# Optimization experiments

Hardware: AMD Instinct MI355X
Metric: run time of the kernel (lower is better)

Reference implementation:

```python
import jax, jax.numpy as jnp
import numpy as np

B, L, H = 2, 2048, 2048
DI, N, DTR, K = 4096, 16, 128, 4  # intermediate, state, dt_rank, conv kernel


def setup_inputs() -> dict:
    key = jax.random.key(0)
    ks = jax.random.split(key, 8)
    x = jax.random.normal(ks[0], (B, L, H), jnp.float32)
    in_proj_w = jax.random.normal(ks[1], (2 * DI, H), jnp.float32) * 0.02
    conv1d_w = jax.random.normal(ks[2], (DI, 1, K), jnp.float32) * 0.1
    conv1d_b = jnp.zeros((DI,), jnp.float32)
    x_proj_w = jax.random.normal(ks[3], (DTR + 2 * N, DI), jnp.float32) * 0.02
    bound = DTR ** -0.5
    dt_proj_w = jax.random.uniform(ks[4], (DI, DTR), jnp.float32, -bound, bound)
    # faithful dt bias init: inverse-softplus of dt ~ Uniform-log[0.001, 0.1]
    dt = jnp.exp(jax.random.uniform(ks[5], (DI,), jnp.float32)
                 * (np.log(0.1) - np.log(0.001)) + np.log(0.001))
    dt = jnp.clip(dt, 1e-4)
    dt_proj_b = dt + jnp.log(-jnp.expm1(-dt))
    A_log = jnp.log(jnp.broadcast_to(jnp.arange(1, N + 1, dtype=jnp.float32), (DI, N)))
    D = jnp.ones((DI,), jnp.float32)
    out_proj_w = jax.random.normal(ks[6], (H, DI), jnp.float32) * 0.02
    return dict(x=x, in_proj_w=in_proj_w, conv1d_w=conv1d_w, conv1d_b=conv1d_b,
                x_proj_w=x_proj_w, dt_proj_w=dt_proj_w, dt_proj_b=dt_proj_b,
                A_log=A_log, D=D, out_proj_w=out_proj_w)


def _mamba_forward(x, in_proj_w, conv1d_w, conv1d_b, x_proj_w,
                   dt_proj_w, dt_proj_b, A_log, D, out_proj_w):
    # in_proj -> split into ssm input and gate (res)
    x_and_res = jnp.einsum('blh,eh->ble', x, in_proj_w)          # [B,L,2*DI]
    xi, res = jnp.split(x_and_res, 2, axis=-1)                    # [B,L,DI] each

    # depthwise causal conv1d (kernel K, left-pad K-1, truncated to L)
    xc = jnp.transpose(xi, (0, 2, 1))                             # [B,DI,L]
    xc = jax.lax.conv_general_dilated(
        xc, conv1d_w, window_strides=(1,), padding=((K - 1, 0),),
        dimension_numbers=('NCH', 'OIH', 'NCH'), feature_group_count=DI)
    xc = xc + conv1d_b[None, :, None]
    u = jax.nn.silu(jnp.transpose(xc, (0, 2, 1)))                 # [B,L,DI]

    # selective SSM parameters
    A = -jnp.exp(A_log.astype(jnp.float32))                       # [DI,N]
    x_dbl = jnp.einsum('bld,ed->ble', u, x_proj_w)                # [B,L,DTR+2N]
    dlt, Bm, Cm = jnp.split(x_dbl, [DTR, DTR + N], axis=-1)
    delta = jax.nn.softplus(jnp.einsum('blr,dr->bld', dlt, dt_proj_w) + dt_proj_b)

    # selective scan over time; carry h: [B,DI,N]
    def step(h, inp):
        d_t, B_t, C_t, u_t = inp                                  # [B,DI],[B,N],[B,N],[B,DI]
        dA = jnp.exp(d_t[:, :, None] * A)                         # [B,DI,N]
        h = dA * h + d_t[:, :, None] * B_t[:, None, :] * u_t[:, :, None]
        y_t = jnp.einsum('bdn,bn->bd', h, C_t)
        return h, y_t

    xs = (jnp.transpose(delta, (1, 0, 2)), jnp.transpose(Bm, (1, 0, 2)),
          jnp.transpose(Cm, (1, 0, 2)), jnp.transpose(u, (1, 0, 2)))
    h0 = jnp.zeros((x.shape[0], DI, N), jnp.float32)
    _, ys = jax.lax.scan(step, h0, xs)                            # ys: [L,B,DI]
    y = jnp.transpose(ys, (1, 0, 2)) + u * D.astype(jnp.float32)  # skip via D

    y = y * jax.nn.silu(res)                                      # gate
    return jnp.einsum('bld,hd->blh', y, out_proj_w)               # [B,L,H]


def reference(x, in_proj_w, conv1d_w, conv1d_b, x_proj_w,
              dt_proj_w, dt_proj_b, A_log, D, out_proj_w):
    return _mamba_forward(x, in_proj_w, conv1d_w, conv1d_b, x_proj_w,
                          dt_proj_w, dt_proj_b, A_log, D, out_proj_w)
```

## Files before the change

### kernel.cpp

```cpp
#include <hip/hip_runtime.h>
#include <hip/hip_bf16.h>
#include <stdint.h>

#define DEV static __device__ __forceinline__

typedef __attribute__((ext_vector_type(8))) short short8;
typedef __attribute__((ext_vector_type(4))) float f32x4;
typedef __attribute__((address_space(3))) void lds_void;
typedef __attribute__((address_space(1))) void glb_void;

constexpr int CB = 2, CL = 2048, CH = 2048, CDI = 4096, CN = 16, CDTR = 128;
constexpr int BLR = CB * CL;
constexpr int NC = 32, LC = 64;
constexpr int KSL = 8;

DEV ushort f2b(float f) {
  union { float f; uint32_t u; } v; v.f = f;
  uint32_t u = v.u;
  return (ushort)((u + 0x7fffu + ((u >> 16) & 1u)) >> 16);
}
DEV float b2f(ushort b) {
  union { uint32_t u; float f; } v; v.u = ((uint32_t)b) << 16;
  return v.f;
}
DEV void gload16(const ushort* g, ushort* l) {
  __builtin_amdgcn_global_load_lds((const glb_void*)g, (lds_void*)l, 16, 0, 0);
}
DEV f32x4 mfma16(short8 a, short8 b, f32x4 c) {
  return __builtin_amdgcn_mfma_f32_16x16x32_bf16(a, b, c, 0, 0, 0);
}

__global__ void cast_kernel(const float* __restrict__ in, ushort* __restrict__ out, int n4) {
  int i = blockIdx.x * blockDim.x + threadIdx.x;
  if (i >= n4) return;
  float4 v = *(const float4*)(in + (size_t)i * 4);
  *(ushort4*)(out + (size_t)i * 4) = make_ushort4(f2b(v.x), f2b(v.y), f2b(v.z), f2b(v.w));
}

__global__ void cast_pad_xproj_kernel(const float* __restrict__ in, ushort* __restrict__ out) {
  int i = blockIdx.x * blockDim.x + threadIdx.x;
  if (i >= (256 * 4096 / 4)) return;
  int idx = i * 4;
  int r = idx >> 12;
  ushort4 o;
  if (r < 160) {
    float4 v = *(const float4*)(in + idx);
    o = make_ushort4(f2b(v.x), f2b(v.y), f2b(v.z), f2b(v.w));
  } else {
    o = make_ushort4(0, 0, 0, 0);
  }
  *(ushort4*)(out + idx) = o;
}

__global__ void conv_silu_kernel(const ushort* __restrict__ xr, const float* __restrict__ w,
                                 const float* __restrict__ bias, ushort* __restrict__ u) {
  int t = blockIdx.x * blockDim.x + threadIdx.x;
  if (t >= BLR * CDI / 2) return;
  int d2 = t & (CDI / 2 - 1);
  int bl = t >> 11;
  int l = bl & (CL - 1);
  int d = d2 << 1;
  float4 w0 = *(const float4*)(w + (size_t)d * 4);
  float4 w1 = *(const float4*)(w + (size_t)d * 4 + 4);
  float wa0[4] = {w0.x, w0.y, w0.z, w0.w};
  float wa1[4] = {w1.x, w1.y, w1.z, w1.w};
  float a0 = bias[d], a1 = bias[d + 1];
#pragma unroll
  for (int k = 0; k < 4; ++k) {
    int ls = l - 3 + k;
    if (ls >= 0) {
      ushort2 xv = *(const ushort2*)(xr + (size_t)(bl - 3 + k) * 8192 + d);
      a0 = fmaf(wa0[k], b2f(xv.x), a0);
      a1 = fmaf(wa1[k], b2f(xv.y), a1);
    }
  }
  float s0 = a0 / (1.f + __expf(-a0));
  float s1 = a1 / (1.f + __expf(-a1));
  *(ushort2*)(u + (size_t)bl * 4096 + d) = make_ushort2(f2b(s0), f2b(s1));
}

template<int EPI>
__global__ __launch_bounds__(256, 4)
void gemm_bt_kernel(const ushort* __restrict__ A, const ushort* __restrict__ Bw,
                    void* __restrict__ Cp, const float* __restrict__ bias,
                    int M, int N, int K) {
  __shared__ ushort sA[128 * 32];
  __shared__ ushort sB[128 * 32];
  const int tid = threadIdx.x;
  const int bm = blockIdx.x, bn = blockIdx.y;
  const int w = tid >> 6, l = tid & 63;
  const int wr = w >> 1, wc = w & 1;
  const int q = l >> 4, r = l & 15;

  f32x4 acc[4][4] = {};

  const ushort* Ab = A + (size_t)bm * 128 * K;
  const ushort* Bb = Bw + (size_t)bn * 128 * K;
  const int nk = K >> 5;
  for (int kt = 0; kt < nk; ++kt) {
    const int k0 = kt << 5;
#pragma unroll
    for (int i = 0; i < 2; ++i) {
      const int chunk = i * 256 + tid;
      const int row = chunk >> 2;
      const int cofs = (chunk & 3) << 3;
      gload16(Ab + (size_t)row * K + k0 + cofs, sA + chunk * 8);
      gload16(Bb + (size_t)row * K + k0 + cofs, sB + chunk * 8);
    }
    __syncthreads();
    short8 af[4], bfg[4];
#pragma unroll
    for (int i = 0; i < 4; ++i) {
      af[i]  = *(const short8*)(sA + (wr * 64 + i * 16 + r) * 32 + q * 8);
      bfg[i] = *(const short8*)(sB + (wc * 64 + i * 16 + r) * 32 + q * 8);
    }
#pragma unroll
    for (int i = 0; i < 4; ++i)
#pragma unroll
      for (int j = 0; j < 4; ++j)
        acc[i][j] = mfma16(af[i], bfg[j], acc[i][j]);
    __syncthreads();
  }

  const int m0 = bm * 128 + wr * 64;
  const int n0 = bn * 128 + wc * 64;
#pragma unroll
  for (int i = 0; i < 4; ++i) {
#pragma unroll
    for (int j = 0; j < 4; ++j) {
#pragma unroll
      for (int v = 0; v < 4; ++v) {
        const int grow = m0 + i * 16 + q * 4 + v;
        const int gcol = n0 + j * 16 + r;
        const float val = acc[i][j][v];
        if (EPI == 0) {
          ((ushort*)Cp)[(size_t)grow * N + gcol] = f2b(val);
        } else if (EPI == 1) {
          ((float*)Cp)[(size_t)grow * N + gcol] = val;
        } else {
          float xv = val + bias[gcol];
          float sp = xv > 20.f ? xv : log1pf(__expf(xv));
          ((ushort*)Cp)[(size_t)grow * N + gcol] = f2b(sp);
        }
      }
    }
  }
}

template<int EPI>
__global__ __launch_bounds__(512, 1)
void gemm256p_kernel(const ushort* __restrict__ A, const ushort* __restrict__ Bw,
                     void* __restrict__ Cp, int N, int K) {
  __shared__ ushort sA[2][16384];
  __shared__ ushort sB[2][16384];
  const int tid = threadIdx.x;
  const int bm = blockIdx.x, bn = blockIdx.y;
  const int wid = tid >> 6, l = tid & 63;
  const int wr = wid >> 2, wc = wid & 3;
  const int q = l >> 4, r = l & 15;
  const int rx = r & 7;
  const int nt = K >> 6;

  const ushort* Ab = A + (size_t)bm * 256 * K;
  const ushort* Bb = Bw + (size_t)bn * 256 * K;

  const int srow = tid >> 3;
  const int sxor = (tid & 7) ^ (srow & 7);

  auto stageA = [&](int T, int j) {
    const int Ts = (T < nt) ? T : (nt - 1);
    gload16(Ab + (size_t)(j * 64 + srow) * K + Ts * 64 + sxor * 8,
            &sA[T & 1][0] + j * 4096 + tid * 8);
  };
  auto stageB = [&](int T, int j) {
    const int Ts = (T < nt) ? T : (nt - 1);
    gload16(Bb + (size_t)(j * 64 + srow) * K + Ts * 64 + sxor * 8,
            &sB[T & 1][0] + j * 4096 + tid * 8);
  };

  const int sl0 = (q ^ rx) * 8;
  const int sl1 = ((4 + q) ^ rx) * 8;

  f32x4 acc[8][4] = {};

  stageA(0, 1); stageA(0, 3);
  stageB(0, 0); stageA(0, 0);
  stageB(0, 2); stageA(0, 2);
  stageB(0, 1); stageB(0, 3);
  stageA(1, 1); stageA(1, 3);
  asm volatile("s_waitcnt vmcnt(2)" ::: "memory");
  __builtin_amdgcn_s_barrier();

#define PHASE(M0, M1, S0, S1, LAST)                                        \
  {                                                                        \
    const int ra0 = (wr * 128 + (M0) * 16 + r) * 64;                       \
    const int ra1 = (wr * 128 + (M1) * 16 + r) * 64;                       \
    short8 a00 = *(const short8*)(At + ra0 + sl0);                         \
    short8 a01 = *(const short8*)(At + ra0 + sl1);                         \
    short8 a10 = *(const short8*)(At + ra1 + sl0);                         \
    short8 a11 = *(const short8*)(At + ra1 + sl1);                         \
    S0; S1;                                                                \
    if (LAST) asm volatile("s_waitcnt vmcnt(2)" ::: "memory");             \
    __builtin_amdgcn_s_barrier();                                          \
    asm volatile("s_waitcnt lgkmcnt(0)" ::: "memory");                     \
    __builtin_amdgcn_sched_barrier(0);                                     \
    __builtin_amdgcn_s_setprio(1);                                         \
    _Pragma("unroll")                                                      \
    for (int n = 0; n < 4; ++n) {                                          \
      acc[M0][n] = mfma16(a00, bf[n][0], acc[M0][n]);                      \
      acc[M0][n] = mfma16(a01, bf[n][1], acc[M0][n]);                      \
      acc[M1][n] = mfma16(a10, bf[n][0], acc[M1][n]);                      \
      acc[M1][n] = mfma16(a11, bf[n][1], acc[M1][n]);                      \
    }                                                                      \
    __builtin_amdgcn_s_setprio(0);                                         \
    __builtin_amdgcn_sched_barrier(0);                                     \
    __builtin_amdgcn_s_barrier();                                          \
  }

  for (int t = 0; t < nt; ++t) {
    const ushort* At = &sA[t & 1][0];
    const ushort* Bt = &sB[t & 1][0];
    short8 bf[4][2];
#pragma unroll
    for (int n = 0; n < 4; ++n) {
      const int br = (wc * 64 + n * 16 + r) * 64;
      bf[n][0] = *(const short8*)(Bt + br + sl0);
      bf[n][1] = *(const short8*)(Bt + br + sl1);
    }
    PHASE(6, 7, stageB(t + 1, 0), stageA(t + 1, 0), false)
    PHASE(4, 5, stageB(t + 1, 2), stageA(t + 1, 2), false)
    PHASE(2, 3, stageB(t + 1, 1), stageB(t + 1, 3), false)
    PHASE(0, 1, stageA(t + 2, 1), stageA(t + 2, 3), true)
  }
#undef PHASE

  const int m0g = bm * 256 + wr * 128;
  const int n0g = bn * 256 + wc * 64;
#pragma unroll
  for (int m = 0; m < 8; ++m)
#pragma unroll
    for (int n = 0; n < 4; ++n)
#pragma unroll
      for (int v = 0; v < 4; ++v) {
        const int grow = m0g + m * 16 + q * 4 + v;
        const int gcol = n0g + n * 16 + r;
        if (EPI == 0) ((ushort*)Cp)[(size_t)grow * N + gcol] = f2b(acc[m][n][v]);
        else          ((float*)Cp)[(size_t)grow * N + gcol]  = acc[m][n][v];
      }
}

__global__ __launch_bounds__(256, 4)
void gemm_btk_kernel(const ushort* __restrict__ A, const ushort* __restrict__ Bw,
                     float* __restrict__ Cpart, int N, int Ktot, int Ksl) {
  __shared__ ushort sA[128 * 32];
  __shared__ ushort sB[128 * 32];
  const int tid = threadIdx.x;
  const int bm = blockIdx.x, bn = blockIdx.y, z = blockIdx.z;
  const int w = tid >> 6, l = tid & 63;
  const int wr = w >> 1, wc = w & 1;
  const int q = l >> 4, r = l & 15;

  f32x4 acc[4][4] = {};

  const ushort* Ab = A + (size_t)bm * 128 * Ktot + z * Ksl;
  const ushort* Bb = Bw + (size_t)bn * 128 * Ktot + z * Ksl;
  const int nk = Ksl >> 5;
  for (int kt = 0; kt < nk; ++kt) {
    const int k0 = kt << 5;
#pragma unroll
    for (int i = 0; i < 2; ++i) {
      const int chunk = i * 256 + tid;
      const int row = chunk >> 2;
      const int cofs = (chunk & 3) << 3;
      gload16(Ab + (size_t)row * Ktot + k0 + cofs, sA + chunk * 8);
      gload16(Bb + (size_t)row * Ktot + k0 + cofs, sB + chunk * 8);
    }
    __syncthreads();
    short8 af[4], bfg[4];
#pragma unroll
    for (int i = 0; i < 4; ++i) {
      af[i]  = *(const short8*)(sA + (wr * 64 + i * 16 + r) * 32 + q * 8);
      bfg[i] = *(const short8*)(sB + (wc * 64 + i * 16 + r) * 32 + q * 8);
    }
#pragma unroll
    for (int i = 0; i < 4; ++i)
#pragma unroll
      for (int j = 0; j < 4; ++j)
        acc[i][j] = mfma16(af[i], bfg[j], acc[i][j]);
    __syncthreads();
  }

  float* Cz = Cpart + (size_t)z * BLR * N;
  const int m0 = bm * 128 + wr * 64;
  const int n0 = bn * 128 + wc * 64;
#pragma unroll
  for (int i = 0; i < 4; ++i)
#pragma unroll
    for (int j = 0; j < 4; ++j)
#pragma unroll
      for (int v = 0; v < 4; ++v)
        Cz[(size_t)(m0 + i * 16 + q * 4 + v) * N + (n0 + j * 16 + r)] = acc[i][j][v];
}

__global__ __launch_bounds__(256)
void reduce_xdbl_kernel(const float* __restrict__ part, float* __restrict__ xdbl,
                        ushort* __restrict__ dlt) {
  const int i = blockIdx.x * 256 + threadIdx.x;
  const int idx = i * 4;
  const int row = idx >> 8, col = idx & 255;
  float4 s = make_float4(0.f, 0.f, 0.f, 0.f);
#pragma unroll
  for (int z = 0; z < KSL; ++z) {
    float4 v = *(const float4*)(part + (size_t)z * BLR * 256 + idx);
    s.x += v.x; s.y += v.y; s.z += v.z; s.w += v.w;
  }
  *(float4*)(xdbl + idx) = s;
  if (col < 128) {
    *(ushort4*)(dlt + (size_t)row * 128 + col) =
        make_ushort4(f2b(s.x), f2b(s.y), f2b(s.z), f2b(s.w));
  }
}

__global__ __launch_bounds__(256)
void scan_pass1_kernel(const ushort* __restrict__ delta_bf, const ushort* __restrict__ u_bf,
                       const float* __restrict__ xdbl, const float* __restrict__ A_log,
                       float* __restrict__ Hc, float* __restrict__ Ssum) {
  __shared__ float4 sB[LC * 4];
  const int blk = blockIdx.x;
  const int dblk = blk & 15, bc = blk >> 4;
  const int b = bc & (CB - 1), c = bc >> 1;
  const int tid = threadIdx.x;
  const int d = dblk * 256 + tid;
  const size_t rowbase = (size_t)b * CL + c * LC;

  {
    const int rr = tid >> 2, seg = tid & 3;
    sB[tid] = *(const float4*)(xdbl + (rowbase + rr) * 256 + 128 + seg * 4);
  }
  __syncthreads();

  float Ae[16];
#pragma unroll
  for (int n = 0; n < 16; ++n) Ae[n] = -__expf(A_log[(size_t)d * CN + n]);
  float h[16] = {};
  float S = 0.f;
  for (int t = 0; t < LC; ++t) {
    const float dl = b2f(delta_bf[(rowbase + t) * 4096 + d]);
    const float uu = b2f(u_bf[(rowbase + t) * 4096 + d]);
    const float du = dl * uu;
    S += dl;
#pragma unroll
    for (int q = 0; q < 4; ++q) {
      float4 bq = sB[t * 4 + q];
      h[q * 4 + 0] = __expf(Ae[q * 4 + 0] * dl) * h[q * 4 + 0] + du * bq.x;
      h[q * 4 + 1] = __expf(Ae[q * 4 + 1] * dl) * h[q * 4 + 1] + du * bq.y;
      h[q * 4 + 2] = __expf(Ae[q * 4 + 2] * dl) * h[q * 4 + 2] + du * bq.z;
      h[q * 4 + 3] = __expf(Ae[q * 4 + 3] * dl) * h[q * 4 + 3] + du * bq.w;
    }
  }
  float4* Hp = (float4*)(Hc + ((((size_t)c * CB + b) * CDI + d) << 4));
#pragma unroll
  for (int q = 0; q < 4; ++q)
    Hp[q] = make_float4(h[q * 4 + 0], h[q * 4 + 1], h[q * 4 + 2], h[q * 4 + 3]);
  Ssum[((size_t)c * CB + b) * CDI + d] = S;
}

__global__ __launch_bounds__(256)
void scan_pass2_kernel(float* __restrict__ Hc, const float* __restrict__ Ssum,
                       const float* __restrict__ A_log) {
  const int t = blockIdx.x * 256 + threadIdx.x;
  const int n = t & 15, d = (t >> 4) & (CDI - 1), b = t >> 16;
  const float Ae = -__expf(A_log[(size_t)d * CN + n]);
  float h = 0.f;
  for (int c = 1; c < NC; ++c) {
    const size_t idxp = ((size_t)(c - 1) * CB + b) * CDI + d;
    const float P = __expf(Ae * Ssum[idxp]);
    h = P * h + Hc[idxp * 16 + n];
    Hc[idxp * 16 + n] = h;
  }
}

__global__ __launch_bounds__(256)
void scan_pass3_kernel(const ushort* __restrict__ delta_bf, const ushort* __restrict__ u_bf,
                       const float* __restrict__ xdbl, const ushort* __restrict__ xr,
                       const float* __restrict__ A_log, const float* __restrict__ Dvec,
                       const float* __restrict__ Hc, ushort* __restrict__ ybf) {
  __shared__ float4 sB[LC * 4];
  __shared__ float4 sC[LC * 4];
  const int blk = blockIdx.x;
  const int dblk = blk & 15, bc = blk >> 4;
  const int b = bc & (CB - 1), c = bc >> 1;
  const int tid = threadIdx.x;
  const int d = dblk * 256 + tid;
  const size_t rowbase = (size_t)b * CL + c * LC;

  {
    const int rr = tid >> 2, seg = tid & 3;
    sB[tid] = *(const float4*)(xdbl + (rowbase + rr) * 256 + 128 + seg * 4);
    sC[tid] = *(const float4*)(xdbl + (rowbase + rr) * 256 + 144 + seg * 4);
  }
  __syncthreads();

  float Ae[16];
#pragma unroll
  for (int n = 0; n < 16; ++n) Ae[n] = -__expf(A_log[(size_t)d * CN + n]);
  float h[16];
  if (c == 0) {
#pragma unroll
    for (int n = 0; n < 16; ++n) h[n] = 0.f;
  } else {
    const float4* Hp = (const float4*)(Hc + ((((size_t)(c - 1) * CB + b) * CDI + d) << 4));
#pragma unroll
    for (int q = 0; q < 4; ++q) {
      float4 hv = Hp[q];
      h[q * 4 + 0] = hv.x; h[q * 4 + 1] = hv.y; h[q * 4 + 2] = hv.z; h[q * 4 + 3] = hv.w;
    }
  }
  const float Dd = Dvec[d];
  for (int t = 0; t < LC; ++t) {
    const float dl = b2f(delta_bf[(rowbase + t) * 4096 + d]);
    const float uu = b2f(u_bf[(rowbase + t) * 4096 + d]);
    const float du = dl * uu;
    float y = 0.f;
#pragma unroll
    for (int q = 0; q < 4; ++q) {
      float4 bq = sB[t * 4 + q];
      float4 cq = sC[t * 4 + q];
      h[q * 4 + 0] = __expf(Ae[q * 4 + 0] * dl) * h[q * 4 + 0] + du * bq.x;
      h[q * 4 + 1] = __expf(Ae[q * 4 + 1] * dl) * h[q * 4 + 1] + du * bq.y;
      h[q * 4 + 2] = __expf(Ae[q * 4 + 2] * dl) * h[q * 4 + 2] + du * bq.z;
      h[q * 4 + 3] = __expf(Ae[q * 4 + 3] * dl) * h[q * 4 + 3] + du * bq.w;
      y = fmaf(h[q * 4 + 0], cq.x, y);
      y = fmaf(h[q * 4 + 1], cq.y, y);
      y = fmaf(h[q * 4 + 2], cq.z, y);
      y = fmaf(h[q * 4 + 3], cq.w, y);
    }
    const float res = b2f(xr[(rowbase + t) * 8192 + 4096 + d]);
    const float sres = res / (1.f + __expf(-res));
    ybf[(rowbase + t) * 4096 + d] = f2b((y + uu * Dd) * sres);
  }
}

extern "C" void kernel_launch(void* const* d_in, const int* in_sizes, int n_in,
                              void* d_out, int out_size, void* d_ws, size_t ws_size,
                              hipStream_t stream) {
  (void)in_sizes; (void)n_in; (void)out_size; (void)ws_size;
  const float* x       = (const float*)d_in[0];
  const float* in_w    = (const float*)d_in[1];
  const float* conv_w  = (const float*)d_in[2];
  const float* conv_b  = (const float*)d_in[3];
  const float* xproj_w = (const float*)d_in[4];
  const float* dt_w    = (const float*)d_in[5];
  const float* dt_b    = (const float*)d_in[6];
  const float* A_log   = (const float*)d_in[7];
  const float* Dvec    = (const float*)d_in[8];
  const float* out_w   = (const float*)d_in[9];
  float* out = (float*)d_out;
  char* ws = (char*)d_ws;
  const size_t MB = 1u << 20;

  ushort* xb    = (ushort*)(ws);
  float*  Hc    = (float*)(ws);
  ushort* wout  = (ushort*)(ws);
  ushort* wb1   = (ushort*)(ws + 16 * MB);
  ushort* u_bf  = (ushort*)(ws + 16 * MB);
  ushort* xr    = (ushort*)(ws + 48 * MB);
  float*  part  = (float*)(ws + 112 * MB);
  ushort* delta = (ushort*)(ws + 112 * MB);
  ushort* ybf   = (ushort*)(ws + 144 * MB);
  float*  xdbl  = (float*)(ws + 176 * MB);
  ushort* dlt   = (ushort*)(ws + 180 * MB);
  ushort* wxp   = (ushort*)(ws + 181 * MB);
  ushort* wdt   = (ushort*)(ws + 183 * MB);
  float*  Ssum  = (float*)(ws + 184 * MB);

  auto cast = [&](const float* in, ushort* o, int n) {
    cast_kernel<<<(n / 4 + 255) / 256, 256, 0, stream>>>(in, o, n / 4);
  };

  cast(x, xb, BLR * CH);
  cast(in_w, wb1, 2 * CDI * CH);
  gemm256p_kernel<0><<<dim3(BLR / 256, (2 * CDI) / 256), 512, 0, stream>>>(
      xb, wb1, xr, 2 * CDI, CH);
  conv_silu_kernel<<<(BLR * CDI / 2) / 256, 256, 0, stream>>>(xr, conv_w, conv_b, u_bf);
  cast_pad_xproj_kernel<<<(256 * 4096 / 4) / 256, 256, 0, stream>>>(xproj_w, wxp);
  gemm_btk_kernel<<<dim3(BLR / 128, 2, KSL), 256, 0, stream>>>(
      u_bf, wxp, part, 256, CDI, CDI / KSL);
  reduce_xdbl_kernel<<<(BLR * 256 / 4) / 256, 256, 0, stream>>>(part, xdbl, dlt);
  cast(dt_w, wdt, CDI * CDTR);
  gemm_bt_kernel<2><<<dim3(BLR / 128, CDI / 128), 256, 0, stream>>>(
      dlt, wdt, delta, dt_b, BLR, CDI, CDTR);
  scan_pass1_kernel<<<NC * CB * (CDI / 256), 256, 0, stream>>>(
      delta, u_bf, xdbl, A_log, Hc, Ssum);
  scan_pass2_kernel<<<(CB * CDI * CN) / 256, 256, 0, stream>>>(Hc, Ssum, A_log);
  scan_pass3_kernel<<<NC * CB * (CDI / 256), 256, 0, stream>>>(
      delta, u_bf, xdbl, xr, A_log, Dvec, Hc, ybf);
  cast(out_w, wout, CH * CDI);
  gemm_bt_kernel<1><<<dim3(BLR / 128, CH / 128), 256, 0, stream>>>(
      ybf, wout, out, nullptr, BLR, CH, CDI);
}
```

Measured before the change: 547.2 us.

## Vectorize conv_silu to 8 channels per thread and restructure in_proj GEMM phases

The depthwise conv+SiLU kernel now handles 8 channels per thread with 16-byte loads and stores instead of 2 channels, which cuts instruction count and narrow memory accesses. The 256x256 in_proj GEMM merges its four per-iteration phases into two, each loading four A fragments and issuing 32 MFMAs between barriers, so it synchronises half as often. Launch bounds move from 1 to 2 blocks per CU to allow more occupancy. This raises register pressure, and with 128 KB of LDS per block the second block may not fit at all.

After: 572.8 us. 1.05x slower.

```diff
diff --git a/kernel.cpp b/kernel.cpp
--- a/kernel.cpp
+++ b/kernel.cpp
@@ -55,28 +55,39 @@
 __global__ void conv_silu_kernel(const ushort* __restrict__ xr, const float* __restrict__ w,
                                  const float* __restrict__ bias, ushort* __restrict__ u) {
   int t = blockIdx.x * blockDim.x + threadIdx.x;
-  if (t >= BLR * CDI / 2) return;
-  int d2 = t & (CDI / 2 - 1);
-  int bl = t >> 11;
-  int l = bl & (CL - 1);
-  int d = d2 << 1;
-  float4 w0 = *(const float4*)(w + (size_t)d * 4);
-  float4 w1 = *(const float4*)(w + (size_t)d * 4 + 4);
-  float wa0[4] = {w0.x, w0.y, w0.z, w0.w};
-  float wa1[4] = {w1.x, w1.y, w1.z, w1.w};
-  float a0 = bias[d], a1 = bias[d + 1];
+  if (t >= BLR * CDI / 8) return;
+  const int d8 = (t & (CDI / 8 - 1)) << 3;
+  const int bl = t >> 9;
+  const int l = bl & (CL - 1);
+  float a[8];
+  {
+    float4 b0 = *(const float4*)(bias + d8);
+    float4 b1 = *(const float4*)(bias + d8 + 4);
+    a[0] = b0.x; a[1] = b0.y; a[2] = b0.z; a[3] = b0.w;
+    a[4] = b1.x; a[5] = b1.y; a[6] = b1.z; a[7] = b1.w;
+  }
+  float wk[8][4];
+#pragma unroll
+  for (int j = 0; j < 8; ++j) {
+    float4 wj = *(const float4*)(w + (size_t)(d8 + j) * 4);
+    wk[j][0] = wj.x; wk[j][1] = wj.y; wk[j][2] = wj.z; wk[j][3] = wj.w;
+  }
 #pragma unroll
   for (int k = 0; k < 4; ++k) {
-    int ls = l - 3 + k;
-    if (ls >= 0) {
-      ushort2 xv = *(const ushort2*)(xr + (size_t)(bl - 3 + k) * 8192 + d);
-      a0 = fmaf(wa0[k], b2f(xv.x), a0);
-      a1 = fmaf(wa1[k], b2f(xv.y), a1);
-    }
-  }
-  float s0 = a0 / (1.f + __expf(-a0));
-  float s1 = a1 / (1.f + __expf(-a1));
-  *(ushort2*)(u + (size_t)bl * 4096 + d) = make_ushort2(f2b(s0), f2b(s1));
+    if (l - 3 + k >= 0) {
+      short8 xv = *(const short8*)(xr + (size_t)(bl - 3 + k) * 8192 + d8);
+#pragma unroll
+      for (int j = 0; j < 8; ++j)
+        a[j] = fmaf(wk[j][k], b2f((ushort)xv[j]), a[j]);
+    }
+  }
+  short8 o;
+#pragma unroll
+  for (int j = 0; j < 8; ++j) {
+    float s = a[j] / (1.f + __expf(-a[j]));
+    o[j] = (short)f2b(s);
+  }
+  *(short8*)(u + (size_t)bl * 4096 + d8) = o;
 }
 
 template<int EPI>
@@ -148,7 +159,7 @@
 }
 
 template<int EPI>
-__global__ __launch_bounds__(512, 1)
+__global__ __launch_bounds__(512, 2)
 void gemm256p_kernel(const ushort* __restrict__ A, const ushort* __restrict__ Bw,
                      void* __restrict__ Cp, int N, int K) {
   __shared__ ushort sA[2][16384];
@@ -191,32 +202,6 @@
   asm volatile("s_waitcnt vmcnt(2)" ::: "memory");
   __builtin_amdgcn_s_barrier();
 
-#define PHASE(M0, M1, S0, S1, LAST)                                        \
-  {                                                                        \
-    const int ra0 = (wr * 128 + (M0) * 16 + r) * 64;                       \
-    const int ra1 = (wr * 128 + (M1) * 16 + r) * 64;                       \
-    short8 a00 = *(const short8*)(At + ra0 + sl0);                         \
-    short8 a01 = *(const short8*)(At + ra0 + sl1);                         \
-    short8 a10 = *(const short8*)(At + ra1 + sl0);                         \
-    short8 a11 = *(const short8*)(At + ra1 + sl1);                         \
-    S0; S1;                                                                \
-    if (LAST) asm volatile("s_waitcnt vmcnt(2)" ::: "memory");             \
-    __builtin_amdgcn_s_barrier();                                          \
-    asm volatile("s_waitcnt lgkmcnt(0)" ::: "memory");                     \
-    __builtin_amdgcn_sched_barrier(0);                                     \
-    __builtin_amdgcn_s_setprio(1);                                         \
-    _Pragma("unroll")                                                      \
-    for (int n = 0; n < 4; ++n) {                                          \
-      acc[M0][n] = mfma16(a00, bf[n][0], acc[M0][n]);                      \
-      acc[M0][n] = mfma16(a01, bf[n][1], acc[M0][n]);                      \
-      acc[M1][n] = mfma16(a10, bf[n][0], acc[M1][n]);                      \
-      acc[M1][n] = mfma16(a11, bf[n][1], acc[M1][n]);                      \
-    }                                                                      \
-    __builtin_amdgcn_s_setprio(0);                                         \
-    __builtin_amdgcn_sched_barrier(0);                                     \
-    __builtin_amdgcn_s_barrier();                                          \
-  }
-
   for (int t = 0; t < nt; ++t) {
     const ushort* At = &sA[t & 1][0];
     const ushort* Bt = &sB[t & 1][0];
@@ -227,12 +212,58 @@
       bf[n][0] = *(const short8*)(Bt + br + sl0);
       bf[n][1] = *(const short8*)(Bt + br + sl1);
     }
-    PHASE(6, 7, stageB(t + 1, 0), stageA(t + 1, 0), false)
-    PHASE(4, 5, stageB(t + 1, 2), stageA(t + 1, 2), false)
-    PHASE(2, 3, stageB(t + 1, 1), stageB(t + 1, 3), false)
-    PHASE(0, 1, stageA(t + 2, 1), stageA(t + 2, 3), true)
-  }
-#undef PHASE
+    {
+      short8 a[4][2];
+#pragma unroll
+      for (int mm = 0; mm < 4; ++mm) {
+        const int ra = (wr * 128 + (4 + mm) * 16 + r) * 64;
+        a[mm][0] = *(const short8*)(At + ra + sl0);
+        a[mm][1] = *(const short8*)(At + ra + sl1);
+      }
+      stageB(t + 1, 0); stageA(t + 1, 0);
+      stageB(t + 1, 2); stageA(t + 1, 2);
+      __builtin_amdgcn_s_barrier();
+      asm volatile("s_waitcnt lgkmcnt(0)" ::: "memory");
+      __builtin_amdgcn_sched_barrier(0);
+      __builtin_amdgcn_s_setprio(1);
+#pragma unroll
+      for (int mm = 0; mm < 4; ++mm)
+#pragma unroll
+        for (int n = 0; n < 4; ++n) {
+          acc[4 + mm][n] = mfma16(a[mm][0], bf[n][0], acc[4 + mm][n]);
+          acc[4 + mm][n] = mfma16(a[mm][1], bf[n][1], acc[4 + mm][n]);
+        }
+      __builtin_amdgcn_s_setprio(0);
+      __builtin_amdgcn_sched_barrier(0);
+      __builtin_amdgcn_s_barrier();
+    }
+    {
+      short8 a[4][2];
+#pragma unroll
+      for (int mm = 0; mm < 4; ++mm) {
+        const int ra = (wr * 128 + mm * 16 + r) * 64;
+        a[mm][0] = *(const short8*)(At + ra + sl0);
+        a[mm][1] = *(const short8*)(At + ra + sl1);
+      }
+      stageB(t + 1, 1); stageB(t + 1, 3);
+      stageA(t + 2, 1); stageA(t + 2, 3);
+      asm volatile("s_waitcnt vmcnt(2)" ::: "memory");
+      __builtin_amdgcn_s_barrier();
+      asm volatile("s_waitcnt lgkmcnt(0)" ::: "memory");
+      __builtin_amdgcn_sched_barrier(0);
+      __builtin_amdgcn_s_setprio(1);
+#pragma unroll
+      for (int mm = 0; mm < 4; ++mm)
+#pragma unroll
+        for (int n = 0; n < 4; ++n) {
+          acc[mm][n] = mfma16(a[mm][0], bf[n][0], acc[mm][n]);
+          acc[mm][n] = mfma16(a[mm][1], bf[n][1], acc[mm][n]);
+        }
+      __builtin_amdgcn_s_setprio(0);
+      __builtin_amdgcn_sched_barrier(0);
+      __builtin_amdgcn_s_barrier();
+    }
+  }
 
   const int m0g = bm * 256 + wr * 128;
   const int n0g = bn * 256 + wc * 64;
@@ -482,7 +513,7 @@
   cast(in_w, wb1, 2 * CDI * CH);
   gemm256p_kernel<0><<<dim3(BLR / 256, (2 * CDI) / 256), 512, 0, stream>>>(
       xb, wb1, xr, 2 * CDI, CH);
-  conv_silu_kernel<<<(BLR * CDI / 2) / 256, 256, 0, stream>>>(xr, conv_w, conv_b, u_bf);
+  conv_silu_kernel<<<(BLR * CDI / 8) / 256, 256, 0, stream>>>(xr, conv_w, conv_b, u_bf);
   cast_pad_xproj_kernel<<<(256 * 4096 / 4) / 256, 256, 0, stream>>>(xproj_w, wxp);
   gemm_btk_kernel<<<dim3(BLR / 128, 2, KSL), 256, 0, stream>>>(
       u_bf, wxp, part, 256, CDI, CDI / KSL);
```
